# Kernel optimization log

Measured on AMD Instinct MI355X. Metric: run time of the kernel, lower is better.

The kernel has to match this reference:

```python
import jax, jax.numpy as jnp
import numpy as np
from jax import lax

PATCH_SIZE = 14
BLUR_W_L, BLUR_PAD_L, BLUR_REPEATS_L = 5, 2, 5
BLUR_W_U, BLUR_PAD_U, BLUR_REPEATS_U = 7, 3, 3
TOPK_RATIO = 0.001
EPS = 1e-12


def setup_inputs() -> dict:
    key = jax.random.key(0)
    k1, k2, k3, k4 = jax.random.split(key, 4)
    B, N, C = 16, 1024, 768  # 448/14 = 32 -> 32*32 = 1024 patches
    return {
        "middle_patch": jax.random.normal(k1, (B, N, C), dtype=jnp.float32),
        "last_patch": jax.random.normal(k2, (B, N, C), dtype=jnp.float32),
        "predicted_middle_patch": jax.random.normal(k3, (B, N, C), dtype=jnp.float32),
        "predicted_last_patch": jax.random.normal(k4, (B, N, C), dtype=jnp.float32),
        "out_h": 448,
        "out_w": 448,
    }


def _l2_normalize(x):
    # matches torch F.normalize(dim=-1): x / max(||x||_2, 1e-12)
    n = jnp.sqrt(jnp.sum(x * x, axis=-1, keepdims=True))
    return x / jnp.maximum(n, EPS)


def _conv_blur(x, k, pad):
    # x: (B,1,H,W); uniform kxk box filter, stride 1, same-size output
    w = jnp.full((1, 1, k, k), 1.0 / (k * k), dtype=x.dtype)
    return lax.conv_general_dilated(
        x, w, window_strides=(1, 1), padding=[(pad, pad), (pad, pad)],
        dimension_numbers=("NCHW", "OIHW", "NCHW"))


def _blur(x):
    for _ in range(BLUR_REPEATS_L):
        x = _conv_blur(x, BLUR_W_L, BLUR_PAD_L)
    for _ in range(BLUR_REPEATS_U):
        x = _conv_blur(x, BLUR_W_U, BLUR_PAD_U)
    return x


def reference(middle_patch, last_patch, predicted_middle_patch,
              predicted_last_patch, out_h, out_w):
    b = middle_patch.shape[0]
    h, w = int(out_h), int(out_w)
    h_p, w_p = h // PATCH_SIZE, w // PATCH_SIZE

    middle_anom = jnp.sqrt(jnp.sum(
        (_l2_normalize(predicted_middle_patch) - _l2_normalize(middle_patch)) ** 2, axis=-1))
    last_anom = jnp.sqrt(jnp.sum(
        (_l2_normalize(predicted_last_patch) - _l2_normalize(last_patch)) ** 2, axis=-1))
    combined = middle_anom * last_anom  # (B, h_p*w_p)

    anomaly_map = combined.reshape(b, 1, h_p, w_p)
    # bilinear upsample with half-pixel centers == torch align_corners=False
    anomaly_map = jax.image.resize(anomaly_map, (b, 1, h, w), method="bilinear")
    anomaly_map = _blur(anomaly_map)

    n = h * w
    k = max(1, int(n * TOPK_RATIO))
    topk_vals, _ = lax.top_k(anomaly_map.reshape(b, n), k)
    pred_score = jnp.mean(topk_vals, axis=1)
    return anomaly_map, pred_score
```

## Files before the change

kernel.cpp:

```cpp
#include <hip/hip_runtime.h>

constexpr int C = 768;
constexpr int NPATCH = 1024;
constexpr int H = 448, W = 448;
constexpr int HW = H * W;
constexpr int TOPK = 200;
constexpr float EPS = 1e-12f;

constexpr int HBITS = 13;
constexpr int HBINS = 1 << HBITS;
constexpr int HSHIFT = 18;
constexpr int CSTRIDE = 64;

typedef float f32x4 __attribute__((ext_vector_type(4)));

__device__ __forceinline__ float dotv(const f32x4 a, const f32x4 b) {
    return a.x * b.x + a.y * b.y + a.z * b.z + a.w * b.w;
}

__global__ __launch_bounds__(256, 4) void anom_kernel(
    const float* __restrict__ m, const float* __restrict__ l,
    const float* __restrict__ pm, const float* __restrict__ pl,
    float* __restrict__ combined, uint4* __restrict__ zp, int n4, int rows) {
    if (blockIdx.x < 132) {
        int z = blockIdx.x * 256 + threadIdx.x;
        if (z < n4) zp[z] = make_uint4(0u, 0u, 0u, 0u);
    }
    int wid = (int)((blockIdx.x * blockDim.x + threadIdx.x) >> 6);
    int lane = threadIdx.x & 63;
    if (wid >= rows) return;
    size_t base = (size_t)wid * C;
    const f32x4* A = (const f32x4*)(m + base);
    const f32x4* B = (const f32x4*)(pm + base);
    const f32x4* Cc = (const f32x4*)(l + base);
    const f32x4* D = (const f32x4*)(pl + base);

    f32x4 a0 = __builtin_nontemporal_load(A + lane);
    f32x4 a1 = __builtin_nontemporal_load(A + lane + 64);
    f32x4 a2 = __builtin_nontemporal_load(A + lane + 128);
    f32x4 b0 = __builtin_nontemporal_load(B + lane);
    f32x4 b1 = __builtin_nontemporal_load(B + lane + 64);
    f32x4 b2 = __builtin_nontemporal_load(B + lane + 128);
    f32x4 c0 = __builtin_nontemporal_load(Cc + lane);
    f32x4 c1 = __builtin_nontemporal_load(Cc + lane + 64);
    f32x4 c2 = __builtin_nontemporal_load(Cc + lane + 128);
    f32x4 d0 = __builtin_nontemporal_load(D + lane);
    f32x4 d1 = __builtin_nontemporal_load(D + lane + 64);
    f32x4 d2 = __builtin_nontemporal_load(D + lane + 128);

    float mm = dotv(a0, a0) + dotv(a1, a1) + dotv(a2, a2);
    float pp = dotv(b0, b0) + dotv(b1, b1) + dotv(b2, b2);
    float mp = dotv(a0, b0) + dotv(a1, b1) + dotv(a2, b2);
    float ll = dotv(c0, c0) + dotv(c1, c1) + dotv(c2, c2);
    float qq = dotv(d0, d0) + dotv(d1, d1) + dotv(d2, d2);
    float lq = dotv(c0, d0) + dotv(c1, d1) + dotv(c2, d2);

#pragma unroll
    for (int off = 32; off > 0; off >>= 1) {
        mm += __shfl_xor(mm, off);
        pp += __shfl_xor(pp, off);
        mp += __shfl_xor(mp, off);
        ll += __shfl_xor(ll, off);
        qq += __shfl_xor(qq, off);
        lq += __shfl_xor(lq, off);
    }
    if (lane == 0) {
        float rm = 1.0f / fmaxf(sqrtf(mm), EPS);
        float rp = 1.0f / fmaxf(sqrtf(pp), EPS);
        float rl = 1.0f / fmaxf(sqrtf(ll), EPS);
        float rq = 1.0f / fmaxf(sqrtf(qq), EPS);
        float d2m = fmaxf(mm * rm * rm - 2.f * mp * rm * rp + pp * rp * rp, 0.f);
        float d2l = fmaxf(ll * rl * rl - 2.f * lq * rl * rq + qq * rq * rq, 0.f);
        combined[wid] = sqrtf(d2m) * sqrtf(d2l);
    }
}


__device__ void build_G(float (*g)[449], int tid) {
    int i = tid & 31;
    int chunk = tid >> 5;
    int x0 = chunk * 32;

#pragma unroll 1
    for (int k = 0; k < 32; ++k) {
        int x = x0 + k;
        float sx = (x + 0.5f) * (1.0f / 14.0f) - 0.5f;
        float f0 = floorf(sx);
        float fx = sx - f0;
        int q0 = (int)f0;
        int q0c = min(max(q0, 0), 31);
        int q1c = min(max(q0 + 1, 0), 31);
        float w = 0.f;
        if (q0c == i) w += 1.0f - fx;
        if (q1c == i) w += fx;
        g[i][x] = w;
    }
    __syncthreads();

#pragma unroll 1
    for (int pass = 0; pass < 8; ++pass) {
        float win[38];
#pragma unroll
        for (int j = 0; j < 38; ++j) {
            int xw = x0 - 3 + j;
            win[j] = (xw >= 0 && xw < 448) ? g[i][xw] : 0.f;
        }
        float out[32];
        if (pass < 5) {
            constexpr float inv5 = 1.0f / 5.0f;
#pragma unroll
            for (int k = 0; k < 32; ++k)
                out[k] = (win[k + 1] + win[k + 2] + win[k + 3] + win[k + 4] +
                          win[k + 5]) * inv5;
        } else {
            constexpr float inv7 = 1.0f / 7.0f;
#pragma unroll
            for (int k = 0; k < 32; ++k)
                out[k] = (win[k] + win[k + 1] + win[k + 2] + win[k + 3] +
                          win[k + 4] + win[k + 5] + win[k + 6]) * inv7;
        }
        __syncthreads();
#pragma unroll
        for (int k = 0; k < 32; ++k) g[i][x0 + k] = out[k];
        __syncthreads();
    }
}

__global__ __launch_bounds__(448) void stageA_kernel(
    const float* __restrict__ comb, float* __restrict__ Gout,
    float* __restrict__ T) {
    __shared__ float g[32][449];
    __shared__ float combT[32][32];
    int b = blockIdx.x;
    int x = threadIdx.x;
    const float* cb = comb + (size_t)b * 1024;
    for (int idx = x; idx < 1024; idx += 448)
        combT[idx & 31][idx >> 5] = cb[idx];

    build_G(g, x);

    f32x4 acc[8];
#pragma unroll
    for (int k = 0; k < 8; ++k) acc[k] = (f32x4){0.f, 0.f, 0.f, 0.f};
#pragma unroll 1
    for (int j = 0; j < 32; ++j) {
        float w = g[j][x];
#pragma unroll
        for (int k = 0; k < 8; ++k) {
            f32x4 c = *(const f32x4*)&combT[j][k * 4];
            acc[k] += c * w;
        }
    }
    float* t = T + ((size_t)b * 448 + x) * 32;
#pragma unroll
    for (int k = 0; k < 8; ++k) *(f32x4*)(t + k * 4) = acc[k];

    if (b == 0) {
        for (int idx = x; idx < 448 * 32; idx += 448)
            Gout[idx] = g[idx & 31][idx >> 5];
    }
}

__global__ __launch_bounds__(448) void stageB_kernel(
    const float* __restrict__ T, const float* __restrict__ G,
    float* __restrict__ map, unsigned* __restrict__ hist) {
    __shared__ float gband[28][32];
    __shared__ unsigned lh[HBINS];
    int b = blockIdx.x >> 4;
    int band = blockIdx.x & 15;
    int x = threadIdx.x;

    for (int i = x; i < HBINS; i += 448) lh[i] = 0;
    for (int i = x; i < 28 * 32; i += 448)
        gband[i >> 5][i & 31] = G[(band * 28 + (i >> 5)) * 32 + (i & 31)];
    f32x4 t[8];
    const float* tp = T + ((size_t)b * 448 + x) * 32;
#pragma unroll
    for (int k = 0; k < 8; ++k) t[k] = *(const f32x4*)(tp + k * 4);
    __syncthreads();

    float* out = map + (size_t)b * HW + (size_t)band * 28 * W;
#pragma unroll 1
    for (int yy = 0; yy < 28; ++yy) {
        f32x4 a = {0.f, 0.f, 0.f, 0.f};
#pragma unroll
        for (int k = 0; k < 8; ++k) {
            f32x4 g4 = *(const f32x4*)&gband[yy][k * 4];
            a += g4 * t[k];
        }
        float v = a.x + a.y + a.z + a.w;
        out[yy * W + x] = v;
        atomicAdd(&lh[__float_as_uint(v) >> HSHIFT], 1u);
    }
    __syncthreads();
    unsigned* gh = hist + (size_t)b * HBINS;
    for (int i = x; i < HBINS; i += 448) {
        unsigned c = lh[i];
        if (c) atomicAdd(&gh[i], c);
    }
}


__global__ __launch_bounds__(256) void select_kernel(
    const unsigned* __restrict__ hist, int* __restrict__ selbin) {
    int b = blockIdx.x;
    const unsigned* gh = hist + (size_t)b * HBINS;
    constexpr int CHUNK = HBINS / 256;
    __shared__ unsigned ss[257];
    __shared__ unsigned cs2[33];
    __shared__ int sh_base, sh_k;
    int tid = threadIdx.x;
    unsigned s = 0;
#pragma unroll
    for (int j = 0; j < CHUNK; ++j) s += gh[tid * CHUNK + j];
    ss[tid] = s;
    if (tid == 0) ss[256] = 0;
    __syncthreads();
#pragma unroll
    for (int st = 1; st < 256; st <<= 1) {
        unsigned add = (tid + st < 256) ? ss[tid + st] : 0u;
        __syncthreads();
        ss[tid] += add;
        __syncthreads();
    }
    if ((int)ss[tid] >= TOPK && (int)ss[tid + 1] < TOPK) {
        sh_base = tid * CHUNK;
        sh_k = TOPK - (int)ss[tid + 1];
    }
    __syncthreads();
    int base = sh_base, kk = sh_k;
    if (tid < 32) cs2[tid] = gh[base + tid];
    if (tid == 0) cs2[32] = 0;
    __syncthreads();
#pragma unroll
    for (int st = 1; st < 32; st <<= 1) {
        unsigned add = (tid < 32 && tid + st < 32) ? cs2[tid + st] : 0u;
        __syncthreads();
        if (tid < 32) cs2[tid] += add;
        __syncthreads();
    }
    if (tid < 32 && (int)cs2[tid] >= kk && (int)cs2[tid + 1] < kk)
        selbin[b * CSTRIDE] = base + tid;
}

__global__ __launch_bounds__(256) void compact_kernel(
    const float* __restrict__ map, const int* __restrict__ selbin,
    int* __restrict__ ccount, float* __restrict__ cand) {
    int tid = threadIdx.x;
    size_t base = (size_t)blockIdx.x * 1024;
    int b = (int)(base / HW);
    int sb = selbin[b * CSTRIDE];
    const uint4* u4 = (const uint4*)(((const unsigned*)map) + base);
    uint4 v = u4[tid];
    unsigned take0 = ((int)(v.x >> HSHIFT) >= sb);
    unsigned take1 = ((int)(v.y >> HSHIFT) >= sb);
    unsigned take2 = ((int)(v.z >> HSHIFT) >= sb);
    unsigned take3 = ((int)(v.w >> HSHIFT) >= sb);
    int c = (int)(take0 + take1 + take2 + take3);

    __shared__ int blkcnt, blkbase;
    if (tid == 0) blkcnt = 0;
    __syncthreads();
    int pos = 0;
    if (c) pos = atomicAdd(&blkcnt, c);
    __syncthreads();
    if (tid == 0 && blkcnt > 0)
        blkbase = atomicAdd(&ccount[b * CSTRIDE], blkcnt);
    __syncthreads();
    if (c) {
        float* o = cand + (size_t)b * HW + blkbase + pos;
        if (take0) *o++ = __uint_as_float(v.x);
        if (take1) *o++ = __uint_as_float(v.y);
        if (take2) *o++ = __uint_as_float(v.z);
        if (take3) *o = __uint_as_float(v.w);
    }
}

__global__ __launch_bounds__(256) void topk_kernel(
    const float* __restrict__ cand, const int* __restrict__ ccount,
    float* __restrict__ score) {
    int b = blockIdx.x;
    const float* s = cand + (size_t)b * HW;
    const unsigned* u = (const unsigned*)s;
    int M = ccount[b * CSTRIDE];
    __shared__ unsigned hist[256];
    __shared__ unsigned ss[257];
    __shared__ unsigned sh_prefix;
    __shared__ int sh_k;
    int tid = threadIdx.x;

    unsigned prefix = 0;
    int k = TOPK;
    for (int dgt = 3; dgt >= 0; --dgt) {
        hist[tid] = 0;
        __syncthreads();
        for (int i = tid; i < M; i += 256) {
            unsigned v = u[i];
            bool match = (dgt == 3) || ((v >> (8 * (dgt + 1))) == prefix);
            if (match) atomicAdd(&hist[(v >> (8 * dgt)) & 255u], 1u);
        }
        __syncthreads();
        ss[tid] = hist[tid];
        if (tid == 0) ss[256] = 0;
        __syncthreads();
#pragma unroll
        for (int st = 1; st < 256; st <<= 1) {
            unsigned add = (tid + st < 256) ? ss[tid + st] : 0u;
            __syncthreads();
            ss[tid] += add;
            __syncthreads();
        }
        if ((int)ss[tid] >= k && (int)ss[tid + 1] < k) {
            sh_prefix = (prefix << 8) | (unsigned)tid;
            sh_k = k - (int)ss[tid + 1];
        }
        __syncthreads();
        prefix = sh_prefix;
        k = sh_k;
        __syncthreads();
    }

    float thr = __uint_as_float(prefix);
    float sum = 0.f;
    int cnt = 0;
    for (int i = tid; i < M; i += 256) {
        float v = s[i];
        if (v > thr) { sum += v; cnt++; }
    }
#pragma unroll
    for (int off = 32; off > 0; off >>= 1) {
        sum += __shfl_xor(sum, off);
        cnt += __shfl_xor(cnt, off);
    }
    __shared__ float wsum[4];
    __shared__ int wcnt[4];
    int wv = tid >> 6;
    if ((tid & 63) == 0) { wsum[wv] = sum; wcnt[wv] = cnt; }
    __syncthreads();
    if (tid == 0) {
        float s2 = 0.f;
        int c2 = 0;
        for (int i = 0; i < 4; ++i) { s2 += wsum[i]; c2 += wcnt[i]; }
        score[b] = (s2 + (float)(TOPK - c2) * thr) * (1.0f / TOPK);
    }
}

extern "C" void kernel_launch(void* const* d_in, const int* in_sizes, int n_in,
                              void* d_out, int out_size, void* d_ws, size_t ws_size,
                              hipStream_t stream) {
    const float* mid = (const float*)d_in[0];
    const float* last = (const float*)d_in[1];
    const float* pmid = (const float*)d_in[2];
    const float* plast = (const float*)d_in[3];
    int B = in_sizes[0] / (NPATCH * C);

    float* out_map = (float*)d_out;
    float* out_score = out_map + (size_t)B * HW;

    float* combined = (float*)d_ws;
    int* meta = (int*)((char*)d_ws + 64 * 1024);
    int* ccount = meta;
    int* selbin = meta + 1024;
    unsigned* hist = (unsigned*)((char*)d_ws + 80 * 1024);
    float* Gw = (float*)((char*)d_ws + 592 * 1024);
    float* Tw = (float*)((char*)d_ws + 652 * 1024);
    float* cand = (float*)((char*)d_ws + 1548 * 1024);

    int rows = B * NPATCH;
    int n4 = (528 * 1024) / 16;
    anom_kernel<<<(rows + 3) / 4, 256, 0, stream>>>(
        mid, last, pmid, plast, combined,
        (uint4*)((char*)d_ws + 64 * 1024), n4, rows);

    stageA_kernel<<<B, 448, 0, stream>>>(combined, Gw, Tw);
    stageB_kernel<<<B * 16, 448, 0, stream>>>(Tw, Gw, out_map, hist);

    select_kernel<<<B, 256, 0, stream>>>(hist, selbin);
    int nc = (B * HW) / 1024;
    compact_kernel<<<nc, 256, 0, stream>>>(out_map, selbin, ccount, cand);
    topk_kernel<<<B, 256, 0, stream>>>(cand, ccount, out_score);
}
```

Measured before the change: 100.3 us.

## Fuse stageA into stageB and fold bin selection into compact kernel

Removes two kernel launches. Each stageB block now rebuilds the blur-weight matrix G and recomputes the T column product itself, so the T and G workspaces no longer make a global round trip. The histogram threshold search now runs redundantly inside every compact block instead of in a separate select kernel. This saves launch and serialization overhead but repeats G construction 16 times per image and repeats the 8K-bin scan in thousands of compact blocks.

```diff
diff --git a/kernel.cpp b/kernel.cpp
--- a/kernel.cpp
+++ b/kernel.cpp
@@ -126,57 +126,41 @@
     }
 }
 
-__global__ __launch_bounds__(448) void stageA_kernel(
-    const float* __restrict__ comb, float* __restrict__ Gout,
-    float* __restrict__ T) {
+__global__ __launch_bounds__(448) void stageBG_kernel(
+    const float* __restrict__ comb, float* __restrict__ map,
+    unsigned* __restrict__ hist) {
     __shared__ float g[32][449];
     __shared__ float combT[32][32];
-    int b = blockIdx.x;
-    int x = threadIdx.x;
-    const float* cb = comb + (size_t)b * 1024;
-    for (int idx = x; idx < 1024; idx += 448)
-        combT[idx & 31][idx >> 5] = cb[idx];
-
-    build_G(g, x);
-
-    f32x4 acc[8];
-#pragma unroll
-    for (int k = 0; k < 8; ++k) acc[k] = (f32x4){0.f, 0.f, 0.f, 0.f};
-#pragma unroll 1
-    for (int j = 0; j < 32; ++j) {
-        float w = g[j][x];
-#pragma unroll
-        for (int k = 0; k < 8; ++k) {
-            f32x4 c = *(const f32x4*)&combT[j][k * 4];
-            acc[k] += c * w;
-        }
-    }
-    float* t = T + ((size_t)b * 448 + x) * 32;
-#pragma unroll
-    for (int k = 0; k < 8; ++k) *(f32x4*)(t + k * 4) = acc[k];
-
-    if (b == 0) {
-        for (int idx = x; idx < 448 * 32; idx += 448)
-            Gout[idx] = g[idx & 31][idx >> 5];
-    }
-}
-
-__global__ __launch_bounds__(448) void stageB_kernel(
-    const float* __restrict__ T, const float* __restrict__ G,
-    float* __restrict__ map, unsigned* __restrict__ hist) {
-    __shared__ float gband[28][32];
+    __shared__ float gband[28 * 36];
     __shared__ unsigned lh[HBINS];
     int b = blockIdx.x >> 4;
     int band = blockIdx.x & 15;
     int x = threadIdx.x;
 
+    const float* cb = comb + (size_t)b * 1024;
+    for (int idx = x; idx < 1024; idx += 448)
+        combT[idx & 31][idx >> 5] = cb[idx];
     for (int i = x; i < HBINS; i += 448) lh[i] = 0;
-    for (int i = x; i < 28 * 32; i += 448)
-        gband[i >> 5][i & 31] = G[(band * 28 + (i >> 5)) * 32 + (i & 31)];
+
+    build_G(g, x);
+
     f32x4 t[8];
-    const float* tp = T + ((size_t)b * 448 + x) * 32;
-#pragma unroll
-    for (int k = 0; k < 8; ++k) t[k] = *(const f32x4*)(tp + k * 4);
+#pragma unroll
+    for (int k = 0; k < 8; ++k) t[k] = (f32x4){0.f, 0.f, 0.f, 0.f};
+#pragma unroll 1
+    for (int j = 0; j < 32; ++j) {
+        float w = g[j][x];
+#pragma unroll
+        for (int k = 0; k < 8; ++k) {
+            f32x4 c = *(const f32x4*)&combT[j][k * 4];
+            t[k] += c * w;
+        }
+    }
+
+    for (int idx = x; idx < 28 * 32; idx += 448) {
+        int yy = idx >> 5, i = idx & 31;
+        gband[yy * 36 + i] = g[i][band * 28 + yy];
+    }
     __syncthreads();
 
     float* out = map + (size_t)b * HW + (size_t)band * 28 * W;
@@ -185,7 +169,7 @@
         f32x4 a = {0.f, 0.f, 0.f, 0.f};
 #pragma unroll
         for (int k = 0; k < 8; ++k) {
-            f32x4 g4 = *(const f32x4*)&gband[yy][k * 4];
+            f32x4 g4 = *(const f32x4*)&gband[yy * 36 + k * 4];
             a += g4 * t[k];
         }
         float v = a.x + a.y + a.z + a.w;
@@ -201,55 +185,52 @@
 }
 
 
-__global__ __launch_bounds__(256) void select_kernel(
-    const unsigned* __restrict__ hist, int* __restrict__ selbin) {
-    int b = blockIdx.x;
-    const unsigned* gh = hist + (size_t)b * HBINS;
-    constexpr int CHUNK = HBINS / 256;
-    __shared__ unsigned ss[257];
-    __shared__ unsigned cs2[33];
-    __shared__ int sh_base, sh_k;
-    int tid = threadIdx.x;
-    unsigned s = 0;
-#pragma unroll
-    for (int j = 0; j < CHUNK; ++j) s += gh[tid * CHUNK + j];
-    ss[tid] = s;
-    if (tid == 0) ss[256] = 0;
-    __syncthreads();
-#pragma unroll
-    for (int st = 1; st < 256; st <<= 1) {
-        unsigned add = (tid + st < 256) ? ss[tid + st] : 0u;
-        __syncthreads();
-        ss[tid] += add;
-        __syncthreads();
-    }
-    if ((int)ss[tid] >= TOPK && (int)ss[tid + 1] < TOPK) {
-        sh_base = tid * CHUNK;
-        sh_k = TOPK - (int)ss[tid + 1];
-    }
-    __syncthreads();
-    int base = sh_base, kk = sh_k;
-    if (tid < 32) cs2[tid] = gh[base + tid];
-    if (tid == 0) cs2[32] = 0;
-    __syncthreads();
-#pragma unroll
-    for (int st = 1; st < 32; st <<= 1) {
-        unsigned add = (tid < 32 && tid + st < 32) ? cs2[tid + st] : 0u;
-        __syncthreads();
-        if (tid < 32) cs2[tid] += add;
-        __syncthreads();
-    }
-    if (tid < 32 && (int)cs2[tid] >= kk && (int)cs2[tid + 1] < kk)
-        selbin[b * CSTRIDE] = base + tid;
-}
-
 __global__ __launch_bounds__(256) void compact_kernel(
-    const float* __restrict__ map, const int* __restrict__ selbin,
+    const float* __restrict__ map, const unsigned* __restrict__ hist,
     int* __restrict__ ccount, float* __restrict__ cand) {
     int tid = threadIdx.x;
     size_t base = (size_t)blockIdx.x * 1024;
     int b = (int)(base / HW);
-    int sb = selbin[b * CSTRIDE];
+    const unsigned* gh = hist + (size_t)b * HBINS;
+
+    __shared__ unsigned ss[257];
+    __shared__ unsigned cs2[33];
+    __shared__ int sh_base, sh_k, sh_sb;
+    {
+        unsigned s = 0;
+#pragma unroll
+        for (int j = 0; j < 32; ++j) s += gh[tid * 32 + j];
+        ss[tid] = s;
+        if (tid == 0) ss[256] = 0;
+        __syncthreads();
+#pragma unroll
+        for (int st = 1; st < 256; st <<= 1) {
+            unsigned add = (tid + st < 256) ? ss[tid + st] : 0u;
+            __syncthreads();
+            ss[tid] += add;
+            __syncthreads();
+        }
+        if ((int)ss[tid] >= TOPK && (int)ss[tid + 1] < TOPK)
+            sh_base = tid * 32;
+        __syncthreads();
+        int bse = sh_base;
+        if (tid < 32) cs2[tid] = gh[bse + tid];
+        if (tid == 0) cs2[32] = 0;
+        __syncthreads();
+        int kk = TOPK - (int)ss[bse / 32 + 1];
+#pragma unroll
+        for (int st = 1; st < 32; st <<= 1) {
+            unsigned add = (tid < 32 && tid + st < 32) ? cs2[tid + st] : 0u;
+            __syncthreads();
+            if (tid < 32) cs2[tid] += add;
+            __syncthreads();
+        }
+        if (tid < 32 && (int)cs2[tid] >= kk && (int)cs2[tid + 1] < kk)
+            sh_sb = bse + tid;
+        __syncthreads();
+    }
+    int sb = sh_sb;
+
     const uint4* u4 = (const uint4*)(((const unsigned*)map) + base);
     uint4 v = u4[tid];
     unsigned take0 = ((int)(v.x >> HSHIFT) >= sb);
@@ -360,11 +341,8 @@
     float* combined = (float*)d_ws;
     int* meta = (int*)((char*)d_ws + 64 * 1024);
     int* ccount = meta;
-    int* selbin = meta + 1024;
     unsigned* hist = (unsigned*)((char*)d_ws + 80 * 1024);
-    float* Gw = (float*)((char*)d_ws + 592 * 1024);
-    float* Tw = (float*)((char*)d_ws + 652 * 1024);
-    float* cand = (float*)((char*)d_ws + 1548 * 1024);
+    float* cand = (float*)((char*)d_ws + 592 * 1024);
 
     int rows = B * NPATCH;
     int n4 = (528 * 1024) / 16;
@@ -372,11 +350,9 @@
         mid, last, pmid, plast, combined,
         (uint4*)((char*)d_ws + 64 * 1024), n4, rows);
 
-    stageA_kernel<<<B, 448, 0, stream>>>(combined, Gw, Tw);
-    stageB_kernel<<<B * 16, 448, 0, stream>>>(Tw, Gw, out_map, hist);
-
-    select_kernel<<<B, 256, 0, stream>>>(hist, selbin);
+    stageBG_kernel<<<B * 16, 448, 0, stream>>>(combined, out_map, hist);
+
     int nc = (B * HW) / 1024;
-    compact_kernel<<<nc, 256, 0, stream>>>(out_map, selbin, ccount, cand);
+    compact_kernel<<<nc, 256, 0, stream>>>(out_map, hist, ccount, cand);
     topk_kernel<<<B, 256, 0, stream>>>(cand, ccount, out_score);
 }
```

New measurement: 105.3 us. 1.05x slower.

## Split stageB into finer bands, use warp-aggregated global histogram, fold select into compact

Applied to the files above, without the earlier changes.

StageB now runs 64 bands of 7 rows per image instead of 16 bands of 28 rows, giving four times more blocks and a smaller padded shared-memory tile. The per-block 8K-bin shared histogram is dropped. Each wavefront instead groups lanes that share a bin through ballot/shuffle and issues one global atomic per distinct bin. The separate select kernel is removed, and every compact block recomputes the threshold bin from the histogram itself, trading one launch for redundant scans (3136 blocks each reading 8K bins) and possibly more global atomic contention.

```diff
diff --git a/kernel.cpp b/kernel.cpp
--- a/kernel.cpp
+++ b/kernel.cpp
@@ -164,92 +164,96 @@
 __global__ __launch_bounds__(448) void stageB_kernel(
     const float* __restrict__ T, const float* __restrict__ G,
     float* __restrict__ map, unsigned* __restrict__ hist) {
-    __shared__ float gband[28][32];
-    __shared__ unsigned lh[HBINS];
-    int b = blockIdx.x >> 4;
-    int band = blockIdx.x & 15;
+    __shared__ float gband[7 * 36];
+    int b = blockIdx.x >> 6;
+    int band = blockIdx.x & 63;
     int x = threadIdx.x;
-
-    for (int i = x; i < HBINS; i += 448) lh[i] = 0;
-    for (int i = x; i < 28 * 32; i += 448)
-        gband[i >> 5][i & 31] = G[(band * 28 + (i >> 5)) * 32 + (i & 31)];
+    int lane = x & 63;
+
+    for (int idx = x; idx < 7 * 32; idx += 448)
+        gband[(idx >> 5) * 36 + (idx & 31)] =
+            G[(band * 7 + (idx >> 5)) * 32 + (idx & 31)];
     f32x4 t[8];
     const float* tp = T + ((size_t)b * 448 + x) * 32;
 #pragma unroll
     for (int k = 0; k < 8; ++k) t[k] = *(const f32x4*)(tp + k * 4);
     __syncthreads();
 
-    float* out = map + (size_t)b * HW + (size_t)band * 28 * W;
+    unsigned* gh = hist + (size_t)b * HBINS;
+    float* out = map + (size_t)b * HW + (size_t)band * 7 * W;
 #pragma unroll 1
-    for (int yy = 0; yy < 28; ++yy) {
+    for (int yy = 0; yy < 7; ++yy) {
         f32x4 a = {0.f, 0.f, 0.f, 0.f};
 #pragma unroll
         for (int k = 0; k < 8; ++k) {
-            f32x4 g4 = *(const f32x4*)&gband[yy][k * 4];
+            f32x4 g4 = *(const f32x4*)&gband[yy * 36 + k * 4];
             a += g4 * t[k];
         }
         float v = a.x + a.y + a.z + a.w;
         out[yy * W + x] = v;
-        atomicAdd(&lh[__float_as_uint(v) >> HSHIFT], 1u);
-    }
-    __syncthreads();
-    unsigned* gh = hist + (size_t)b * HBINS;
-    for (int i = x; i < HBINS; i += 448) {
-        unsigned c = lh[i];
-        if (c) atomicAdd(&gh[i], c);
-    }
-}
-
-
-__global__ __launch_bounds__(256) void select_kernel(
-    const unsigned* __restrict__ hist, int* __restrict__ selbin) {
-    int b = blockIdx.x;
-    const unsigned* gh = hist + (size_t)b * HBINS;
-    constexpr int CHUNK = HBINS / 256;
-    __shared__ unsigned ss[257];
-    __shared__ unsigned cs2[33];
-    __shared__ int sh_base, sh_k;
-    int tid = threadIdx.x;
-    unsigned s = 0;
-#pragma unroll
-    for (int j = 0; j < CHUNK; ++j) s += gh[tid * CHUNK + j];
-    ss[tid] = s;
-    if (tid == 0) ss[256] = 0;
-    __syncthreads();
-#pragma unroll
-    for (int st = 1; st < 256; st <<= 1) {
-        unsigned add = (tid + st < 256) ? ss[tid + st] : 0u;
-        __syncthreads();
-        ss[tid] += add;
-        __syncthreads();
-    }
-    if ((int)ss[tid] >= TOPK && (int)ss[tid + 1] < TOPK) {
-        sh_base = tid * CHUNK;
-        sh_k = TOPK - (int)ss[tid + 1];
-    }
-    __syncthreads();
-    int base = sh_base, kk = sh_k;
-    if (tid < 32) cs2[tid] = gh[base + tid];
-    if (tid == 0) cs2[32] = 0;
-    __syncthreads();
-#pragma unroll
-    for (int st = 1; st < 32; st <<= 1) {
-        unsigned add = (tid < 32 && tid + st < 32) ? cs2[tid + st] : 0u;
-        __syncthreads();
-        if (tid < 32) cs2[tid] += add;
-        __syncthreads();
-    }
-    if (tid < 32 && (int)cs2[tid] >= kk && (int)cs2[tid + 1] < kk)
-        selbin[b * CSTRIDE] = base + tid;
-}
+
+        unsigned bin = __float_as_uint(v) >> HSHIFT;
+        bool todo = true;
+        unsigned long long act;
+        while ((act = __ballot(todo)) != 0ull) {
+            int leader = (int)(__ffsll((unsigned long long)act) - 1);
+            unsigned lb = __shfl(bin, leader);
+            bool same = todo && (bin == lb);
+            unsigned long long mset = __ballot(same);
+            if (lane == leader)
+                atomicAdd(&gh[lb], (unsigned)__popcll(mset));
+            if (same) todo = false;
+        }
+    }
+}
+
 
 __global__ __launch_bounds__(256) void compact_kernel(
-    const float* __restrict__ map, const int* __restrict__ selbin,
+    const float* __restrict__ map, const unsigned* __restrict__ hist,
     int* __restrict__ ccount, float* __restrict__ cand) {
     int tid = threadIdx.x;
     size_t base = (size_t)blockIdx.x * 1024;
     int b = (int)(base / HW);
-    int sb = selbin[b * CSTRIDE];
+    const unsigned* gh = hist + (size_t)b * HBINS;
+
+    __shared__ unsigned ss[257];
+    __shared__ unsigned cs2[33];
+    __shared__ int sh_base, sh_sb;
+    {
+        unsigned s = 0;
+#pragma unroll
+        for (int j = 0; j < 32; ++j) s += gh[tid * 32 + j];
+        ss[tid] = s;
+        if (tid == 0) ss[256] = 0;
+        __syncthreads();
+#pragma unroll
+        for (int st = 1; st < 256; st <<= 1) {
+            unsigned add = (tid + st < 256) ? ss[tid + st] : 0u;
+            __syncthreads();
+            ss[tid] += add;
+            __syncthreads();
+        }
+        if ((int)ss[tid] >= TOPK && (int)ss[tid + 1] < TOPK)
+            sh_base = tid * 32;
+        __syncthreads();
+        int bse = sh_base;
+        if (tid < 32) cs2[tid] = gh[bse + tid];
+        if (tid == 0) cs2[32] = 0;
+        __syncthreads();
+        int kk = TOPK - (int)ss[bse / 32 + 1];
+#pragma unroll
+        for (int st = 1; st < 32; st <<= 1) {
+            unsigned add = (tid < 32 && tid + st < 32) ? cs2[tid + st] : 0u;
+            __syncthreads();
+            if (tid < 32) cs2[tid] += add;
+            __syncthreads();
+        }
+        if (tid < 32 && (int)cs2[tid] >= kk && (int)cs2[tid + 1] < kk)
+            sh_sb = bse + tid;
+        __syncthreads();
+    }
+    int sb = sh_sb;
+
     const uint4* u4 = (const uint4*)(((const unsigned*)map) + base);
     uint4 v = u4[tid];
     unsigned take0 = ((int)(v.x >> HSHIFT) >= sb);
@@ -360,7 +364,6 @@
     float* combined = (float*)d_ws;
     int* meta = (int*)((char*)d_ws + 64 * 1024);
     int* ccount = meta;
-    int* selbin = meta + 1024;
     unsigned* hist = (unsigned*)((char*)d_ws + 80 * 1024);
     float* Gw = (float*)((char*)d_ws + 592 * 1024);
     float* Tw = (float*)((char*)d_ws + 652 * 1024);
@@ -373,10 +376,9 @@
         (uint4*)((char*)d_ws + 64 * 1024), n4, rows);
 
     stageA_kernel<<<B, 448, 0, stream>>>(combined, Gw, Tw);
-    stageB_kernel<<<B * 16, 448, 0, stream>>>(Tw, Gw, out_map, hist);
-
-    select_kernel<<<B, 256, 0, stream>>>(hist, selbin);
+    stageB_kernel<<<B * 64, 448, 0, stream>>>(Tw, Gw, out_map, hist);
+
     int nc = (B * HW) / 1024;
-    compact_kernel<<<nc, 256, 0, stream>>>(out_map, selbin, ccount, cand);
+    compact_kernel<<<nc, 256, 0, stream>>>(out_map, hist, ccount, cand);
     topk_kernel<<<B, 256, 0, stream>>>(cand, ccount, out_score);
 }
```

Result: slower. 237.5 us (+136.7%).
